# Optimization experiments

Hardware: AMD Instinct MI355X
Metric: run time of the kernel (lower is better)

The kernel has to match this reference:

```python
import jax, jax.numpy as jnp
import numpy as np

B, C, VC, H, W = 4, 256, 128, 64, 64


def setup_inputs() -> dict:
    key = jax.random.key(0)
    kx, kq, kk, kv = jax.random.split(key, 4)
    # Conv2d 1x1 no-bias weights are just [out_channels, in_channels] matrices.
    s = 1.0 / np.sqrt(C)
    return {
        "x": jax.random.normal(kx, (B, C, H, W), dtype=jnp.float32),
        "Wq": jax.random.uniform(kq, (VC, C), minval=-s, maxval=s, dtype=jnp.float32),
        "Wk": jax.random.uniform(kk, (VC, C), minval=-s, maxval=s, dtype=jnp.float32),
        "Wv": jax.random.uniform(kv, (VC, C), minval=-s, maxval=s, dtype=jnp.float32),
    }


def reference(x, Wq, Wk, Wv):
    # 1x1 convs == per-pixel channel GEMMs
    Q = jnp.einsum('bchw,dc->bdhw', x, Wq)  # [B, VC, H, W]
    K = jnp.einsum('bchw,dc->bdhw', x, Wk)
    V = jnp.einsum('bchw,dc->bdhw', x, Wv)
    b, d, h, w = Q.shape
    # affinity over all spatial pairs: [B, H, W, H, W]
    aff = jnp.einsum('bdij,bdkl->bijkl', Q, K).reshape(b, h, w, h * w)
    aff = jax.nn.softmax(aff, axis=3).reshape(b, h, w, h, w)
    # attention-weighted aggregation of values
    out = jnp.einsum('bijkl,bdkl->bdij', aff, V)  # [B, VC, H, W]
    return out
```

## Files before the change

kernel.cpp:

```cpp
#include <hip/hip_runtime.h>
#include <hip/hip_bf16.h>

#define B_ 4
#define C_ 256
#define D_ 128
#define N_ 4096

typedef float f32x4 __attribute__((ext_vector_type(4)));
typedef short bf16x8 __attribute__((ext_vector_type(8)));
typedef short s16x4 __attribute__((ext_vector_type(4)));
typedef unsigned short u16;
typedef unsigned int u32;

__device__ __forceinline__ u16 f2bf(float f) {
  unsigned u = __float_as_uint(f);
  u += 0x7fffu + ((u >> 16) & 1u);
  return (u16)(u >> 16);
}
__device__ __forceinline__ float bf2f(u16 v) {
  return __uint_as_float(((u32)v) << 16);
}
__device__ __forceinline__ u32 cvt_pk_bf16(float a, float b) {
  u32 r;
  asm("v_cvt_pk_bf16_f32 %0, %1, %2" : "=v"(r) : "v"(a), "v"(b));
  return r;
}

__global__ __launch_bounds__(256) void castw_kernel(
    const float* __restrict__ Wq, const float* __restrict__ Wk,
    const float* __restrict__ Wv, u16* __restrict__ Whi,
    u16* __restrict__ Wlo) {
  const int i = blockIdx.x * 256 + threadIdx.x;
  const int m = i >> 13;
  const int j = (i & 8191) * 4;
  const float* src = (m == 0) ? Wq : (m == 1) ? Wk : Wv;
  const float scale = (m == 0) ? 1.44269504f : 1.0f;
  const float4 v = *(const float4*)(src + j);
  const float vv[4] = {v.x * scale, v.y * scale, v.z * scale, v.w * scale};
  s16x4 h, l;
#pragma unroll
  for (int k = 0; k < 4; ++k) {
    const u16 hb = f2bf(vv[k]);
    h[k] = (short)hb;
    l[k] = (short)f2bf(vv[k] - bf2f(hb));
  }
  *(s16x4*)&Whi[m * 32768 + j] = h;
  *(s16x4*)&Wlo[m * 32768 + j] = l;
}

__global__ __launch_bounds__(256, 3) void proj_kernel(
    const float* __restrict__ x, const u16* __restrict__ Whi,
    const u16* __restrict__ Wlo, u16* __restrict__ Qo, u16* __restrict__ Ko,
    u16* __restrict__ Vt) {
  __shared__ __align__(16) u16 xs_h[32 * 256];
  __shared__ __align__(16) u16 xs_l[32 * 256];

  const int n0 = blockIdx.x * 32;
  const int b = blockIdx.y;
  const int z = blockIdx.z;
  const int t = threadIdx.x;
  const int w = t >> 6, lane = t & 63, g = lane >> 4, c = lane & 15;

  {
    const float* xb = x + ((size_t)b * C_) * N_ + n0;
#pragma unroll
    for (int r = 0; r < 8; ++r) {
      const int id = r * 256 + t;
      const int cr = id >> 3, nq = (id & 7) * 4;
      const float4 v = *(const float4*)(xb + (size_t)cr * N_ + nq);
      const u32 h01 = cvt_pk_bf16(v.x, v.y);
      const u32 h23 = cvt_pk_bf16(v.z, v.w);
      const float r0 = v.x - bf2f((u16)(h01 & 0xffffu));
      const float r1 = v.y - bf2f((u16)(h01 >> 16));
      const float r2 = v.z - bf2f((u16)(h23 & 0xffffu));
      const float r3 = v.w - bf2f((u16)(h23 >> 16));
      const u32 l01 = cvt_pk_bf16(r0, r1);
      const u32 l23 = cvt_pk_bf16(r2, r3);
      const u16 hv[4] = {(u16)(h01 & 0xffffu), (u16)(h01 >> 16),
                         (u16)(h23 & 0xffffu), (u16)(h23 >> 16)};
      const u16 lv[4] = {(u16)(l01 & 0xffffu), (u16)(l01 >> 16),
                         (u16)(l23 & 0xffffu), (u16)(l23 >> 16)};
#pragma unroll
      for (int k2 = 0; k2 < 4; ++k2) {
        const int idx2 = (nq + k2) * 256 + (cr ^ (((nq + k2) & 7) << 3));
        xs_h[idx2] = hv[k2];
        xs_l[idx2] = lv[k2];
      }
    }
  }
  __syncthreads();

  if (w < 2) {
    const size_t wo = (size_t)w * 32768;
    u16* __restrict__ O = (w == 0 ? Qo : Ko) + (size_t)b * N_ * D_;
#pragma unroll 1
    for (int dti = 0; dti < 4; ++dti) {
      const int dt = z * 4 + dti;
      f32x4 a0 = {0.f, 0.f, 0.f, 0.f};
      f32x4 a1 = {0.f, 0.f, 0.f, 0.f};
#pragma unroll 1
      for (int kcb = 0; kcb < 2; ++kcb) {
        bf16x8 wfh[4], wfl[4];
#pragma unroll
        for (int j = 0; j < 4; ++j) {
          const size_t off = wo + (size_t)(dt * 16 + c) * 256 +
                             (kcb * 4 + j) * 32 + g * 8;
          wfh[j] = *(const bf16x8*)&Whi[off];
          wfl[j] = *(const bf16x8*)&Wlo[off];
        }
#pragma unroll
        for (int j = 0; j < 4; ++j) {
          const int kc = kcb * 4 + j;
          const int col = (kc * 32 + g * 8) ^ ((c & 7) << 3);
          const bf16x8 xh0 = *(const bf16x8*)&xs_h[c * 256 + col];
          const bf16x8 xl0 = *(const bf16x8*)&xs_l[c * 256 + col];
          const bf16x8 xh1 = *(const bf16x8*)&xs_h[(16 + c) * 256 + col];
          const bf16x8 xl1 = *(const bf16x8*)&xs_l[(16 + c) * 256 + col];
          a0 = __builtin_amdgcn_mfma_f32_16x16x32_bf16(xh0, wfh[j], a0, 0, 0, 0);
          a0 = __builtin_amdgcn_mfma_f32_16x16x32_bf16(xh0, wfl[j], a0, 0, 0, 0);
          a0 = __builtin_amdgcn_mfma_f32_16x16x32_bf16(xl0, wfh[j], a0, 0, 0, 0);
          a1 = __builtin_amdgcn_mfma_f32_16x16x32_bf16(xh1, wfh[j], a1, 0, 0, 0);
          a1 = __builtin_amdgcn_mfma_f32_16x16x32_bf16(xh1, wfl[j], a1, 0, 0, 0);
          a1 = __builtin_amdgcn_mfma_f32_16x16x32_bf16(xl1, wfh[j], a1, 0, 0, 0);
        }
      }
#pragma unroll
      for (int i = 0; i < 4; ++i) {
        O[(size_t)(n0 + g * 4 + i) * D_ + dt * 16 + c] = f2bf(a0[i]);
        O[(size_t)(n0 + 16 + g * 4 + i) * D_ + dt * 16 + c] = f2bf(a1[i]);
      }
    }
  } else {
    const size_t wo = (size_t)2 * 32768;
    const int d0 = (w - 2) * 64 + z * 32;
    u16* __restrict__ O = Vt + (size_t)b * D_ * N_;
#pragma unroll 1
    for (int dti = 0; dti < 2; ++dti) {
      const int dr = d0 + dti * 16;
      f32x4 a0 = {0.f, 0.f, 0.f, 0.f};
      f32x4 a1 = {0.f, 0.f, 0.f, 0.f};
#pragma unroll 1
      for (int kcb = 0; kcb < 2; ++kcb) {
        bf16x8 wfh[4], wfl[4];
#pragma unroll
        for (int j = 0; j < 4; ++j) {
          const size_t off =
              wo + (size_t)(dr + c) * 256 + (kcb * 4 + j) * 32 + g * 8;
          wfh[j] = *(const bf16x8*)&Whi[off];
          wfl[j] = *(const bf16x8*)&Wlo[off];
        }
#pragma unroll
        for (int j = 0; j < 4; ++j) {
          const int kc = kcb * 4 + j;
          const int col = (kc * 32 + g * 8) ^ ((c & 7) << 3);
          const bf16x8 xh0 = *(const bf16x8*)&xs_h[c * 256 + col];
          const bf16x8 xl0 = *(const bf16x8*)&xs_l[c * 256 + col];
          const bf16x8 xh1 = *(const bf16x8*)&xs_h[(16 + c) * 256 + col];
          const bf16x8 xl1 = *(const bf16x8*)&xs_l[(16 + c) * 256 + col];
          a0 = __builtin_amdgcn_mfma_f32_16x16x32_bf16(wfh[j], xh0, a0, 0, 0, 0);
          a0 = __builtin_amdgcn_mfma_f32_16x16x32_bf16(wfl[j], xh0, a0, 0, 0, 0);
          a0 = __builtin_amdgcn_mfma_f32_16x16x32_bf16(wfh[j], xl0, a0, 0, 0, 0);
          a1 = __builtin_amdgcn_mfma_f32_16x16x32_bf16(wfh[j], xh1, a1, 0, 0, 0);
          a1 = __builtin_amdgcn_mfma_f32_16x16x32_bf16(wfl[j], xh1, a1, 0, 0, 0);
          a1 = __builtin_amdgcn_mfma_f32_16x16x32_bf16(wfh[j], xl1, a1, 0, 0, 0);
        }
      }
#pragma unroll
      for (int i = 0; i < 4; ++i) {
        O[(size_t)(dr + g * 4 + i) * N_ + n0 + c] = f2bf(a0[i]);
        O[(size_t)(dr + g * 4 + i) * N_ + n0 + 16 + c] = f2bf(a1[i]);
      }
    }
  }
}

__device__ __forceinline__ int kIdx(int row, int col) {
  return row * 128 + (col ^ ((row & 7) << 3));
}
__device__ __forceinline__ int vIdx(int d, int col) {
  return d * 64 + (col ^ ((d & 7) << 3));
}
__device__ __forceinline__ int kprm(int q) {
  const int ct = q >> 2, qq = q & 3;
  return ((ct >> 1) << 5) +
         (((qq >> 1) == (ct & 1)) ? (qq << 3) : (((qq ^ 2) << 3) + 4));
}

__global__ __launch_bounds__(256, 2) void attn_kernel(
    const u16* __restrict__ Q, const u16* __restrict__ K,
    const u16* __restrict__ Vt, u16* __restrict__ op,
    float* __restrict__ mb, float* __restrict__ lb,
    float* __restrict__ outf, int qt, int rem, int S) {
  __shared__ __align__(16) u16 lds_k[2][64 * 128];
  __shared__ __align__(16) u16 lds_vt[2][128 * 64];

  const int L = blockIdx.x;
  int qx, b, sid;
  if (((B_ * S) & 7) == 0) {
    const int gpx = (B_ * S) >> 3;
    const int xcd = L & 7, idx = L >> 3;
    const int grp = xcd * gpx + (idx >> 5);
    qx = idx & 31;
    b = grp / S;
    sid = grp - b * S;
  } else {
    qx = L & 31;
    const int r2 = L >> 5;
    b = r2 % B_;
    sid = r2 / B_;
  }
  const int q0 = qx * 128;
  const int NT = qt + (sid < rem ? 1 : 0);
  const int t0 = sid * qt + (sid < rem ? sid : rem);
  const int k0 = t0 * 64;
  const int t = threadIdx.x;
  const int w = t >> 6, lane = t & 63, g = lane >> 4, c = lane & 15;
  const int qw = q0 + w * 32;
  const bool ghi = (g & 2) != 0;

  const u16* __restrict__ Qb = Q + (size_t)b * N_ * D_;
  const u16* __restrict__ Kb = K + (size_t)b * N_ * D_;
  const u16* __restrict__ Vb = Vt + (size_t)b * D_ * N_;

  bf16x8 qf[2][4];
#pragma unroll
  for (int qh = 0; qh < 2; ++qh)
#pragma unroll
    for (int kc = 0; kc < 4; ++kc)
      qf[qh][kc] =
          *(const bf16x8*)&Qb[(size_t)(qw + qh * 16 + c) * D_ + kc * 32 + g * 8];

  f32x4 acc[8][2];
  f32x4 accl[2];
#pragma unroll
  for (int dt = 0; dt < 8; ++dt)
#pragma unroll
    for (int qh = 0; qh < 2; ++qh) acc[dt][qh] = (f32x4){0.f, 0.f, 0.f, 0.f};
  accl[0] = (f32x4){0.f, 0.f, 0.f, 0.f};
  accl[1] = (f32x4){0.f, 0.f, 0.f, 0.f};
  float mrow[2] = {-3.0e38f, -3.0e38f};
  const float THR = 11.5415603f;

  bf16x8 onesv;
#pragma unroll
  for (int j = 0; j < 8; ++j) onesv[j] = (short)0x3F80;

  bf16x8 krg[8], vrg[8];
  auto load_pair = [&](int kbase) {
#pragma unroll
    for (int h = 0; h < 2; ++h)
#pragma unroll
      for (int i = 0; i < 4; ++i) {
        const int idx = i * 256 + t;
        const int kb2 = kbase + h * 64;
        krg[h * 4 + i] =
            *(const bf16x8*)&Kb[(size_t)(kb2 + (idx >> 4)) * D_ + (idx & 15) * 8];
        vrg[h * 4 + i] =
            *(const bf16x8*)&Vb[(size_t)(idx >> 3) * N_ + kb2 + (idx & 7) * 8];
      }
  };
  load_pair(k0);

  auto proc = [&](const u16* kb, const u16* vb) {
    f32x4 s[4][2];
#pragma unroll
    for (int ct = 0; ct < 4; ++ct)
#pragma unroll
      for (int qh = 0; qh < 2; ++qh) s[ct][qh] = (f32x4){0.f, 0.f, 0.f, 0.f};
    __builtin_amdgcn_s_setprio(1);
#pragma unroll
    for (int kc = 0; kc < 4; ++kc) {
#pragma unroll
      for (int ct = 0; ct < 4; ++ct) {
        const bf16x8 kf = *(const bf16x8*)&kb[kIdx(ct * 16 + c, kc * 32 + g * 8)];
        s[ct][0] = __builtin_amdgcn_mfma_f32_16x16x32_bf16(kf, qf[0][kc], s[ct][0], 0, 0, 0);
        s[ct][1] = __builtin_amdgcn_mfma_f32_16x16x32_bf16(kf, qf[1][kc], s[ct][1], 0, 0, 0);
      }
    }
    __builtin_amdgcn_s_setprio(0);

    float pml[2];
#pragma unroll
    for (int qh = 0; qh < 2; ++qh) {
      const float m0 = fmaxf(fmaxf(s[0][qh][0], s[0][qh][1]),
                             fmaxf(s[0][qh][2], s[0][qh][3]));
      const float m1 = fmaxf(fmaxf(s[1][qh][0], s[1][qh][1]),
                             fmaxf(s[1][qh][2], s[1][qh][3]));
      const float m2 = fmaxf(fmaxf(s[2][qh][0], s[2][qh][1]),
                             fmaxf(s[2][qh][2], s[2][qh][3]));
      const float m3 = fmaxf(fmaxf(s[3][qh][0], s[3][qh][1]),
                             fmaxf(s[3][qh][2], s[3][qh][3]));
      pml[qh] = fmaxf(fmaxf(m0, m1), fmaxf(m2, m3));
    }
    const bool need =
        __any((pml[0] > mrow[0] + THR) || (pml[1] > mrow[1] + THR));
    if (need) {
#pragma unroll
      for (int qh = 0; qh < 2; ++qh) {
        float p = pml[qh];
        p = fmaxf(p, __shfl_xor(p, 16));
        p = fmaxf(p, __shfl_xor(p, 32));
        const float mnew = fmaxf(mrow[qh], p);
        const float scl = exp2f(mrow[qh] - mnew);
        mrow[qh] = mnew;
        accl[qh][0] *= scl; accl[qh][1] *= scl;
        accl[qh][2] *= scl; accl[qh][3] *= scl;
#pragma unroll
        for (int dt = 0; dt < 8; ++dt) {
          acc[dt][qh][0] *= scl; acc[dt][qh][1] *= scl;
          acc[dt][qh][2] *= scl; acc[dt][qh][3] *= scl;
        }
      }
    }
#pragma unroll
    for (int qh = 0; qh < 2; ++qh)
#pragma unroll
      for (int ct = 0; ct < 4; ++ct)
#pragma unroll
        for (int i = 0; i < 4; ++i)
          s[ct][qh][i] = exp2f(s[ct][qh][i] - mrow[qh]);

    u32 pfw[2][2][4];
#pragma unroll
    for (int kc = 0; kc < 2; ++kc) {
#pragma unroll
      for (int qh = 0; qh < 2; ++qh) {
        const u32 lo0 = cvt_pk_bf16(s[kc * 2][qh][0], s[kc * 2][qh][1]);
        const u32 lo1 = cvt_pk_bf16(s[kc * 2][qh][2], s[kc * 2][qh][3]);
        const u32 hi0 = cvt_pk_bf16(s[kc * 2 + 1][qh][0], s[kc * 2 + 1][qh][1]);
        const u32 hi1 = cvt_pk_bf16(s[kc * 2 + 1][qh][2], s[kc * 2 + 1][qh][3]);
        pfw[kc][qh][0] = ghi ? hi0 : lo0;
        pfw[kc][qh][1] = ghi ? hi1 : lo1;
        const u32 s0 = ghi ? lo0 : hi0;
        const u32 s1 = ghi ? lo1 : hi1;
        pfw[kc][qh][2] = (u32)__shfl_xor((int)s0, 32);
        pfw[kc][qh][3] = (u32)__shfl_xor((int)s1, 32);
      }
    }

#pragma unroll
    for (int kc = 0; kc < 2; ++kc) {
      union { u32 w2[4]; bf16x8 v; } u0, u1;
#pragma unroll
      for (int j = 0; j < 4; ++j) { u0.w2[j] = pfw[kc][0][j]; u1.w2[j] = pfw[kc][1][j]; }
      __builtin_amdgcn_s_setprio(1);
      accl[0] = __builtin_amdgcn_mfma_f32_16x16x32_bf16(onesv, u0.v, accl[0], 0, 0, 0);
      accl[1] = __builtin_amdgcn_mfma_f32_16x16x32_bf16(onesv, u1.v, accl[1], 0, 0, 0);
#pragma unroll
      for (int dt = 0; dt < 8; ++dt) {
        const bf16x8 vf = *(const bf16x8*)&vb[vIdx(dt * 16 + c, kc * 32 + g * 8)];
        acc[dt][0] = __builtin_amdgcn_mfma_f32_16x16x32_bf16(vf, u0.v, acc[dt][0], 0, 0, 0);
        acc[dt][1] = __builtin_amdgcn_mfma_f32_16x16x32_bf16(vf, u1.v, acc[dt][1], 0, 0, 0);
      }
      __builtin_amdgcn_s_setprio(0);
    }
  };

  for (int kt = 0; kt < NT; kt += 2) {
    __syncthreads();
#pragma unroll
    for (int h = 0; h < 2; ++h)
#pragma unroll
      for (int i = 0; i < 4; ++i) {
        const int idx = i * 256 + t;
        *(bf16x8*)&lds_k[h][kIdx(idx >> 4, (idx & 15) * 8)] = krg[h * 4 + i];
        const int d = idx >> 3, rc = idx & 7;
        const bf16x8 vv = vrg[h * 4 + i];
        s16x4 lo, hi;
        lo[0] = vv[0]; lo[1] = vv[1]; lo[2] = vv[2]; lo[3] = vv[3];
        hi[0] = vv[4]; hi[1] = vv[5]; hi[2] = vv[6]; hi[3] = vv[7];
        *(s16x4*)&lds_vt[h][vIdx(d, kprm(rc * 2))] = lo;
        *(s16x4*)&lds_vt[h][vIdx(d, kprm(rc * 2 + 1))] = hi;
      }
    if (kt + 2 < NT) load_pair(k0 + (kt + 2) * 64);
    __syncthreads();

    proc(&lds_k[0][0], &lds_vt[0][0]);
    proc(&lds_k[1][0], &lds_vt[1][0]);
  }

#pragma unroll
  for (int qh = 0; qh < 2; ++qh) {
    const int n = qw + qh * 16 + c;
    const float lr = accl[qh][0];
    if (mb) {
      u16* __restrict__ ob = op + ((size_t)(sid * B_ + b) * D_) * N_;
#pragma unroll
      for (int dt = 0; dt < 8; ++dt)
#pragma unroll
        for (int i = 0; i < 4; ++i)
          ob[(size_t)(dt * 16 + g * 4 + i) * N_ + n] = f2bf(acc[dt][qh][i]);
      if (g == 0) {
        mb[(size_t)(sid * B_ + b) * N_ + n] = mrow[qh];
        lb[(size_t)(sid * B_ + b) * N_ + n] = lr;
      }
    } else {
      const float linv = 1.0f / lr;
      float* __restrict__ ob = outf + (size_t)b * D_ * N_;
#pragma unroll
      for (int dt = 0; dt < 8; ++dt)
#pragma unroll
        for (int i = 0; i < 4; ++i)
          ob[(size_t)(dt * 16 + g * 4 + i) * N_ + n] = acc[dt][qh][i] * linv;
    }
  }
}

__global__ __launch_bounds__(256) void combine_kernel(
    const u16* __restrict__ op, const float* __restrict__ mbu,
    const float* __restrict__ lbu, float* __restrict__ out, int S) {
  const int idx = blockIdx.x * 256 + threadIdx.x;
  const int n0 = (idx & (N_ / 4 - 1)) * 4;
  const int bd = idx >> 10;
  const int b = bd >> 7, d = bd & (D_ - 1);

  float4 msv[8], lsv[8];
  float M0 = -3e38f, M1 = -3e38f, M2 = -3e38f, M3 = -3e38f;
#pragma unroll
  for (int s = 0; s < 8; ++s)
    if (s < S) {
      msv[s] = *(const float4*)&mbu[(size_t)(s * B_ + b) * N_ + n0];
      lsv[s] = *(const float4*)&lbu[(size_t)(s * B_ + b) * N_ + n0];
      M0 = fmaxf(M0, msv[s].x); M1 = fmaxf(M1, msv[s].y);
      M2 = fmaxf(M2, msv[s].z); M3 = fmaxf(M3, msv[s].w);
    }
  float d0 = 0.f, d1 = 0.f, d2 = 0.f, d3 = 0.f;
  float a0 = 0.f, a1 = 0.f, a2 = 0.f, a3 = 0.f;
#pragma unroll
  for (int s = 0; s < 8; ++s)
    if (s < S) {
      const float w0 = exp2f(msv[s].x - M0);
      const float w1 = exp2f(msv[s].y - M1);
      const float w2 = exp2f(msv[s].z - M2);
      const float w3 = exp2f(msv[s].w - M3);
      d0 += lsv[s].x * w0; d1 += lsv[s].y * w1;
      d2 += lsv[s].z * w2; d3 += lsv[s].w * w3;
      const s16x4 o =
          *(const s16x4*)&op[((size_t)(s * B_ + b) * D_ + d) * N_ + n0];
      a0 += w0 * bf2f((u16)o[0]); a1 += w1 * bf2f((u16)o[1]);
      a2 += w2 * bf2f((u16)o[2]); a3 += w3 * bf2f((u16)o[3]);
    }
  float4 r = {a0 / d0, a1 / d1, a2 / d2, a3 / d3};
  *(float4*)&out[((size_t)b * D_ + d) * N_ + n0] = r;
}

extern "C" void kernel_launch(void* const* d_in, const int* in_sizes, int n_in,
                              void* d_out, int out_size, void* d_ws, size_t ws_size,
                              hipStream_t stream) {
  const float* x  = (const float*)d_in[0];
  const float* Wq = (const float*)d_in[1];
  const float* Wk = (const float*)d_in[2];
  const float* Wv = (const float*)d_in[3];
  float* out = (float*)d_out;

  u16* whi  = (u16*)d_ws;
  u16* wlo  = whi + (size_t)3 * 128 * 256;
  u16* q_ws = wlo + (size_t)3 * 128 * 256;
  u16* k_ws = q_ws + (size_t)B_ * N_ * D_;
  u16* v_ws = k_ws + (size_t)B_ * N_ * D_;

  castw_kernel<<<96, 256, 0, stream>>>(Wq, Wk, Wv, whi, wlo);
  proj_kernel<<<dim3(N_ / 32, B_, 2), 256, 0, stream>>>(x, whi, wlo, q_ws,
                                                        k_ws, v_ws);

  const size_t baseB =
      ((size_t)6 * 128 * 256 + (size_t)3 * B_ * N_ * D_) * 2;
  int S = 0;
  const int cands[3] = {4, 2, 1};
  for (int ci = 0; ci < 3; ++ci) {
    const int cand = cands[ci];
    const size_t need = baseB + (size_t)cand * ((size_t)B_ * D_ * N_ * 2 +
                                                (size_t)2 * B_ * N_ * 4);
    if (ws_size >= need) { S = cand; break; }
  }
  if (S > 1) {
    u16* opb = (u16*)((char*)d_ws + baseB);
    float* mbuf = (float*)(opb + (size_t)S * B_ * D_ * N_);
    float* lbuf = mbuf + (size_t)S * B_ * N_;
    attn_kernel<<<dim3(32 * B_ * S), 256, 0, stream>>>(
        q_ws, k_ws, v_ws, opb, mbuf, lbuf, nullptr, 64 / S, 64 % S, S);
    combine_kernel<<<(B_ * D_ * N_ / 4) / 256, 256, 0, stream>>>(opb, mbuf,
                                                                 lbuf, out, S);
  } else {
    attn_kernel<<<dim3(32 * B_), 256, 0, stream>>>(
        q_ws, k_ws, v_ws, nullptr, nullptr, nullptr, out, 64, 0, 1);
  }
}
```

Before: 97.19 us.

## Drop z-split in projection kernel and compute two d-tiles per iteration

The projection kernel no longer splits output channels across a grid z dimension. Each block now stages x into shared memory once and computes all of Q, K and V for its pixels. Each wave processes two 16-wide d-tiles per iteration with four interleaved accumulators, which reuses the x fragments read from LDS and gives more independent MFMA chains. This removes the duplicate global load and bf16 split of x that the two z-blocks did, at the cost of half as many blocks, more registers (launch bounds lowered to 2) and longer per-block work.

```diff
diff --git a/kernel.cpp b/kernel.cpp
--- a/kernel.cpp
+++ b/kernel.cpp
@@ -48,7 +48,7 @@
   *(s16x4*)&Wlo[m * 32768 + j] = l;
 }
 
-__global__ __launch_bounds__(256, 3) void proj_kernel(
+__global__ __launch_bounds__(256, 2) void proj_kernel(
     const float* __restrict__ x, const u16* __restrict__ Whi,
     const u16* __restrict__ Wlo, u16* __restrict__ Qo, u16* __restrict__ Ko,
     u16* __restrict__ Vt) {
@@ -57,7 +57,6 @@
 
   const int n0 = blockIdx.x * 32;
   const int b = blockIdx.y;
-  const int z = blockIdx.z;
   const int t = threadIdx.x;
   const int w = t >> 6, lane = t & 63, g = lane >> 4, c = lane & 15;
 
@@ -94,19 +93,25 @@
     const size_t wo = (size_t)w * 32768;
     u16* __restrict__ O = (w == 0 ? Qo : Ko) + (size_t)b * N_ * D_;
 #pragma unroll 1
-    for (int dti = 0; dti < 4; ++dti) {
-      const int dt = z * 4 + dti;
-      f32x4 a0 = {0.f, 0.f, 0.f, 0.f};
-      f32x4 a1 = {0.f, 0.f, 0.f, 0.f};
+    for (int dtg = 0; dtg < 4; ++dtg) {
+      f32x4 a00 = {0.f, 0.f, 0.f, 0.f};
+      f32x4 a01 = {0.f, 0.f, 0.f, 0.f};
+      f32x4 a10 = {0.f, 0.f, 0.f, 0.f};
+      f32x4 a11 = {0.f, 0.f, 0.f, 0.f};
+      const int dt0 = dtg * 2, dt1 = dtg * 2 + 1;
 #pragma unroll 1
       for (int kcb = 0; kcb < 2; ++kcb) {
-        bf16x8 wfh[4], wfl[4];
+        bf16x8 w0h[4], w0l[4], w1h[4], w1l[4];
 #pragma unroll
         for (int j = 0; j < 4; ++j) {
-          const size_t off = wo + (size_t)(dt * 16 + c) * 256 +
-                             (kcb * 4 + j) * 32 + g * 8;
-          wfh[j] = *(const bf16x8*)&Whi[off];
-          wfl[j] = *(const bf16x8*)&Wlo[off];
+          const size_t o0 = wo + (size_t)(dt0 * 16 + c) * 256 +
+                            (kcb * 4 + j) * 32 + g * 8;
+          const size_t o1 = wo + (size_t)(dt1 * 16 + c) * 256 +
+                            (kcb * 4 + j) * 32 + g * 8;
+          w0h[j] = *(const bf16x8*)&Whi[o0];
+          w0l[j] = *(const bf16x8*)&Wlo[o0];
+          w1h[j] = *(const bf16x8*)&Whi[o1];
+          w1l[j] = *(const bf16x8*)&Wlo[o1];
         }
 #pragma unroll
         for (int j = 0; j < 4; ++j) {
@@ -116,38 +121,52 @@
           const bf16x8 xl0 = *(const bf16x8*)&xs_l[c * 256 + col];
           const bf16x8 xh1 = *(const bf16x8*)&xs_h[(16 + c) * 256 + col];
           const bf16x8 xl1 = *(const bf16x8*)&xs_l[(16 + c) * 256 + col];
-          a0 = __builtin_amdgcn_mfma_f32_16x16x32_bf16(xh0, wfh[j], a0, 0, 0, 0);
-          a0 = __builtin_amdgcn_mfma_f32_16x16x32_bf16(xh0, wfl[j], a0, 0, 0, 0);
-          a0 = __builtin_amdgcn_mfma_f32_16x16x32_bf16(xl0, wfh[j], a0, 0, 0, 0);
-          a1 = __builtin_amdgcn_mfma_f32_16x16x32_bf16(xh1, wfh[j], a1, 0, 0, 0);
-          a1 = __builtin_amdgcn_mfma_f32_16x16x32_bf16(xh1, wfl[j], a1, 0, 0, 0);
-          a1 = __builtin_amdgcn_mfma_f32_16x16x32_bf16(xl1, wfh[j], a1, 0, 0, 0);
+          a00 = __builtin_amdgcn_mfma_f32_16x16x32_bf16(xh0, w0h[j], a00, 0, 0, 0);
+          a01 = __builtin_amdgcn_mfma_f32_16x16x32_bf16(xh1, w0h[j], a01, 0, 0, 0);
+          a10 = __builtin_amdgcn_mfma_f32_16x16x32_bf16(xh0, w1h[j], a10, 0, 0, 0);
+          a11 = __builtin_amdgcn_mfma_f32_16x16x32_bf16(xh1, w1h[j], a11, 0, 0, 0);
+          a00 = __builtin_amdgcn_mfma_f32_16x16x32_bf16(xh0, w0l[j], a00, 0, 0, 0);
+          a01 = __builtin_amdgcn_mfma_f32_16x16x32_bf16(xh1, w0l[j], a01, 0, 0, 0);
+          a10 = __builtin_amdgcn_mfma_f32_16x16x32_bf16(xh0, w1l[j], a10, 0, 0, 0);
+          a11 = __builtin_amdgcn_mfma_f32_16x16x32_bf16(xh1, w1l[j], a11, 0, 0, 0);
+          a00 = __builtin_amdgcn_mfma_f32_16x16x32_bf16(xl0, w0h[j], a00, 0, 0, 0);
+          a01 = __builtin_amdgcn_mfma_f32_16x16x32_bf16(xl1, w0h[j], a01, 0, 0, 0);
+          a10 = __builtin_amdgcn_mfma_f32_16x16x32_bf16(xl0, w1h[j], a10, 0, 0, 0);
+          a11 = __builtin_amdgcn_mfma_f32_16x16x32_bf16(xl1, w1h[j], a11, 0, 0, 0);
         }
       }
 #pragma unroll
       for (int i = 0; i < 4; ++i) {
-        O[(size_t)(n0 + g * 4 + i) * D_ + dt * 16 + c] = f2bf(a0[i]);
-        O[(size_t)(n0 + 16 + g * 4 + i) * D_ + dt * 16 + c] = f2bf(a1[i]);
+        O[(size_t)(n0 + g * 4 + i) * D_ + dt0 * 16 + c] = f2bf(a00[i]);
+        O[(size_t)(n0 + 16 + g * 4 + i) * D_ + dt0 * 16 + c] = f2bf(a01[i]);
+        O[(size_t)(n0 + g * 4 + i) * D_ + dt1 * 16 + c] = f2bf(a10[i]);
+        O[(size_t)(n0 + 16 + g * 4 + i) * D_ + dt1 * 16 + c] = f2bf(a11[i]);
       }
     }
   } else {
     const size_t wo = (size_t)2 * 32768;
-    const int d0 = (w - 2) * 64 + z * 32;
+    const int dbase = (w - 2) * 64;
     u16* __restrict__ O = Vt + (size_t)b * D_ * N_;
 #pragma unroll 1
-    for (int dti = 0; dti < 2; ++dti) {
-      const int dr = d0 + dti * 16;
-      f32x4 a0 = {0.f, 0.f, 0.f, 0.f};
-      f32x4 a1 = {0.f, 0.f, 0.f, 0.f};
+    for (int dtg = 0; dtg < 2; ++dtg) {
+      f32x4 a00 = {0.f, 0.f, 0.f, 0.f};
+      f32x4 a01 = {0.f, 0.f, 0.f, 0.f};
+      f32x4 a10 = {0.f, 0.f, 0.f, 0.f};
+      f32x4 a11 = {0.f, 0.f, 0.f, 0.f};
+      const int dr0 = dbase + dtg * 32, dr1 = dbase + dtg * 32 + 16;
 #pragma unroll 1
       for (int kcb = 0; kcb < 2; ++kcb) {
-        bf16x8 wfh[4], wfl[4];
+        bf16x8 w0h[4], w0l[4], w1h[4], w1l[4];
 #pragma unroll
         for (int j = 0; j < 4; ++j) {
-          const size_t off =
-              wo + (size_t)(dr + c) * 256 + (kcb * 4 + j) * 32 + g * 8;
-          wfh[j] = *(const bf16x8*)&Whi[off];
-          wfl[j] = *(const bf16x8*)&Wlo[off];
+          const size_t o0 =
+              wo + (size_t)(dr0 + c) * 256 + (kcb * 4 + j) * 32 + g * 8;
+          const size_t o1 =
+              wo + (size_t)(dr1 + c) * 256 + (kcb * 4 + j) * 32 + g * 8;
+          w0h[j] = *(const bf16x8*)&Whi[o0];
+          w0l[j] = *(const bf16x8*)&Wlo[o0];
+          w1h[j] = *(const bf16x8*)&Whi[o1];
+          w1l[j] = *(const bf16x8*)&Wlo[o1];
         }
 #pragma unroll
         for (int j = 0; j < 4; ++j) {
@@ -157,18 +176,26 @@
           const bf16x8 xl0 = *(const bf16x8*)&xs_l[c * 256 + col];
           const bf16x8 xh1 = *(const bf16x8*)&xs_h[(16 + c) * 256 + col];
           const bf16x8 xl1 = *(const bf16x8*)&xs_l[(16 + c) * 256 + col];
-          a0 = __builtin_amdgcn_mfma_f32_16x16x32_bf16(wfh[j], xh0, a0, 0, 0, 0);
-          a0 = __builtin_amdgcn_mfma_f32_16x16x32_bf16(wfl[j], xh0, a0, 0, 0, 0);
-          a0 = __builtin_amdgcn_mfma_f32_16x16x32_bf16(wfh[j], xl0, a0, 0, 0, 0);
-          a1 = __builtin_amdgcn_mfma_f32_16x16x32_bf16(wfh[j], xh1, a1, 0, 0, 0);
-          a1 = __builtin_amdgcn_mfma_f32_16x16x32_bf16(wfl[j], xh1, a1, 0, 0, 0);
-          a1 = __builtin_amdgcn_mfma_f32_16x16x32_bf16(wfh[j], xl1, a1, 0, 0, 0);
+          a00 = __builtin_amdgcn_mfma_f32_16x16x32_bf16(w0h[j], xh0, a00, 0, 0, 0);
+          a01 = __builtin_amdgcn_mfma_f32_16x16x32_bf16(w0h[j], xh1, a01, 0, 0, 0);
+          a10 = __builtin_amdgcn_mfma_f32_16x16x32_bf16(w1h[j], xh0, a10, 0, 0, 0);
+          a11 = __builtin_amdgcn_mfma_f32_16x16x32_bf16(w1h[j], xh1, a11, 0, 0, 0);
+          a00 = __builtin_amdgcn_mfma_f32_16x16x32_bf16(w0l[j], xh0, a00, 0, 0, 0);
+          a01 = __builtin_amdgcn_mfma_f32_16x16x32_bf16(w0l[j], xh1, a01, 0, 0, 0);
+          a10 = __builtin_amdgcn_mfma_f32_16x16x32_bf16(w1l[j], xh0, a10, 0, 0, 0);
+          a11 = __builtin_amdgcn_mfma_f32_16x16x32_bf16(w1l[j], xh1, a11, 0, 0, 0);
+          a00 = __builtin_amdgcn_mfma_f32_16x16x32_bf16(w0h[j], xl0, a00, 0, 0, 0);
+          a01 = __builtin_amdgcn_mfma_f32_16x16x32_bf16(w0h[j], xl1, a01, 0, 0, 0);
+          a10 = __builtin_amdgcn_mfma_f32_16x16x32_bf16(w1h[j], xl0, a10, 0, 0, 0);
+          a11 = __builtin_amdgcn_mfma_f32_16x16x32_bf16(w1h[j], xl1, a11, 0, 0, 0);
         }
       }
 #pragma unroll
       for (int i = 0; i < 4; ++i) {
-        O[(size_t)(dr + g * 4 + i) * N_ + n0 + c] = f2bf(a0[i]);
-        O[(size_t)(dr + g * 4 + i) * N_ + n0 + 16 + c] = f2bf(a1[i]);
+        O[(size_t)(dr0 + g * 4 + i) * N_ + n0 + c] = f2bf(a00[i]);
+        O[(size_t)(dr0 + g * 4 + i) * N_ + n0 + 16 + c] = f2bf(a01[i]);
+        O[(size_t)(dr1 + g * 4 + i) * N_ + n0 + c] = f2bf(a10[i]);
+        O[(size_t)(dr1 + g * 4 + i) * N_ + n0 + 16 + c] = f2bf(a11[i]);
       }
     }
   }
@@ -460,8 +487,8 @@
   u16* v_ws = k_ws + (size_t)B_ * N_ * D_;
 
   castw_kernel<<<96, 256, 0, stream>>>(Wq, Wk, Wv, whi, wlo);
-  proj_kernel<<<dim3(N_ / 32, B_, 2), 256, 0, stream>>>(x, whi, wlo, q_ws,
-                                                        k_ws, v_ws);
+  proj_kernel<<<dim3(N_ / 32, B_), 256, 0, stream>>>(x, whi, wlo, q_ws, k_ws,
+                                                     v_ws);
 
   const size_t baseB =
       ((size_t)6 * 128 * 256 + (size_t)3 * B_ * N_ * D_) * 2;
```

New measurement: 97.24 us. No clear change (+0.1%).
